# Optimization experiments

Hardware: AMD Instinct MI355X
Metric: run time of the kernel (lower is better)

Reference implementation:

```python
import jax, jax.numpy as jnp
import numpy as np

N_NODES = 100000
N_EDGES = 3200000
N_GRAPHS = 1000
F_IN = 3
H = 64


def setup_inputs() -> dict:
    key = jax.random.key(0)
    ks = jax.random.split(key, 12)
    x = jax.random.normal(ks[0], (N_NODES, F_IN), dtype=jnp.float32)
    edge_index = jax.random.randint(ks[1], (2, N_EDGES), 0, N_NODES, dtype=jnp.int64)
    batch = jnp.sort(jax.random.randint(ks[2], (N_NODES,), 0, N_GRAPHS, dtype=jnp.int64))
    def lin(k, fan_in, fan_out):
        bound = 1.0 / np.sqrt(fan_in)
        return jax.random.uniform(k, (fan_in, fan_out), jnp.float32, -bound, bound)
    return {
        "x": x,
        "edge_index": edge_index,
        "batch": batch,
        "eps1": jax.random.uniform(ks[3], (), jnp.float32),
        "eps2": jax.random.uniform(ks[4], (), jnp.float32),
        "eps3": jax.random.uniform(ks[5], (), jnp.float32),
        "W1": lin(ks[6], F_IN, H), "b1": jnp.zeros((H,), jnp.float32),
        "W2": lin(ks[7], H, H),    "b2": jnp.zeros((H,), jnp.float32),
        "W3": lin(ks[8], H, H),    "b3": jnp.zeros((H,), jnp.float32),
        "Wf1": lin(ks[9], H, 10),  "bf1": jnp.zeros((10,), jnp.float32),
        "Wf2": lin(ks[10], 10, 1), "bf2": jnp.zeros((1,), jnp.float32),
    }


def gin_conv(x, src, dst, eps, W, b):
    # GIN: out = nn((1+eps)*x + sum_{j in N(i)} x_j)
    agg = jax.ops.segment_sum(x[src], dst, num_segments=N_NODES)
    h = (1.0 + eps) * x + agg
    return h @ W + b


def reference(x, edge_index, batch, eps1, eps2, eps3, W1, b1, W2, b2, W3, b3, Wf1, bf1, Wf2, bf2):
    src, dst = edge_index[0], edge_index[1]
    h = jax.nn.relu(gin_conv(x, src, dst, eps1, W1, b1))
    h = jax.nn.relu(gin_conv(h, src, dst, eps2, W2, b2))
    h = jax.nn.relu(gin_conv(h, src, dst, eps3, W3, b3))
    # global mean pool over graphs
    sums = jax.ops.segment_sum(h, batch, num_segments=N_GRAPHS)
    counts = jax.ops.segment_sum(jnp.ones((N_NODES, 1), h.dtype), batch, num_segments=N_GRAPHS)
    pooled = sums / jnp.maximum(counts, 1.0)
    out = jax.nn.relu(pooled @ Wf1 + bf1)
    return out @ Wf2 + bf2
```

## Files before the change

kernel.cpp:

```cpp
#include <hip/hip_runtime.h>

#define N_NODES  100000
#define N_EDGES  3200000
#define N_GRAPHS 1000
#define HDIM     64

#define BUCK_LOG 8
#define BUCK_SZ  256
#define NBUCK    ((N_NODES + BUCK_SZ - 1) / BUCK_SZ)
#define CAP      16384
#define BIN_T    256
#define BIN_E    16
#define BIN_CHUNK (BIN_T * BIN_E)
#define CLUS_CAP 12288

typedef __attribute__((ext_vector_type(8))) short short8;
typedef __attribute__((ext_vector_type(4))) float f32x4;
typedef __attribute__((ext_vector_type(4))) int   int4v;


__device__ inline unsigned short f2bf(float v) {
    unsigned int b; __builtin_memcpy(&b, &v, 4);
    return (unsigned short)((b + 0x7FFFu + ((b >> 16) & 1u)) >> 16);
}
__device__ inline float bf2f(unsigned short u) {
    return __uint_as_float(((unsigned int)u) << 16);
}
__device__ inline void sth(unsigned short* p, float v) { *p = f2bf(v); }
__device__ inline float bflo(unsigned int d) { return __uint_as_float(d << 16); }
__device__ inline float bfhi(unsigned int d) { return __uint_as_float(d & 0xFFFF0000u); }

__device__ inline int clampi(int v, int lo, int hi) {
    return v < lo ? lo : (v > hi ? hi : v);
}


__global__ void k_zero(int* __restrict__ p, int n) {
    int i = blockIdx.x * blockDim.x + threadIdx.x;
    if (i < n) p[i] = 0;
}

__global__ void k_curinit(int* __restrict__ gcur) {
    int b = blockIdx.x * blockDim.x + threadIdx.x;
    if (b < NBUCK) gcur[b] = b * CAP;
}

__global__ void k_zrow(uint2* __restrict__ hA, uint2* __restrict__ hB) {
    int t = threadIdx.x;
    uint2 z; z.x = 0u; z.y = 0u;
    if (t < 16)       hA[(size_t)N_NODES * 16 + t] = z;
    else if (t < 32)  hB[(size_t)N_NODES * 16 + (t - 16)] = z;
}


__global__ __launch_bounds__(BIN_T) void k_bin(
        const int* __restrict__ ei, int* __restrict__ gcur,
        unsigned* __restrict__ pairs) {
    __shared__ int hist[NBUCK];
    __shared__ int base[NBUCK];
    for (int i = threadIdx.x; i < NBUCK; i += BIN_T) hist[i] = 0;
    __syncthreads();
    int e0 = blockIdx.x * BIN_CHUNK + threadIdx.x * BIN_E;
    int d[BIN_E], s[BIN_E];
    if (e0 + BIN_E <= N_EDGES) {
        const int4v* s4 = (const int4v*)ei;
        const int4v* d4 = (const int4v*)(ei + N_EDGES);
        #pragma unroll
        for (int q = 0; q < 4; ++q) {
            int4v dv = d4[(e0 >> 2) + q];
            int4v sv = s4[(e0 >> 2) + q];
            #pragma unroll
            for (int j = 0; j < 4; ++j) {
                d[q * 4 + j] = clampi(dv[j], 0, N_NODES - 1);
                s[q * 4 + j] = clampi(sv[j], 0, N_NODES - 1);
            }
        }
        #pragma unroll
        for (int k = 0; k < BIN_E; ++k) atomicAdd(&hist[d[k] >> BUCK_LOG], 1);
    } else {
        for (int k = 0; k < BIN_E; ++k) {
            int e = e0 + k;
            bool v = e < N_EDGES;
            d[k] = v ? clampi(ei[N_EDGES + e], 0, N_NODES - 1) : -1;
            s[k] = v ? clampi(ei[e], 0, N_NODES - 1) : 0;
            if (v) atomicAdd(&hist[d[k] >> BUCK_LOG], 1);
        }
    }
    __syncthreads();
    for (int i = threadIdx.x; i < NBUCK; i += BIN_T) {
        int c = hist[i];
        base[i] = c ? atomicAdd(&gcur[i], c) : 0;
        hist[i] = 0;
    }
    __syncthreads();
    #pragma unroll
    for (int k = 0; k < BIN_E; ++k) {
        if (d[k] >= 0) {
            int bk = d[k] >> BUCK_LOG;
            int r = atomicAdd(&hist[bk], 1);
            int idx = base[bk] + r;
            if (idx < (bk + 1) * CAP)
                pairs[idx] = ((unsigned)(d[k] & (BUCK_SZ - 1)) << 24) | (unsigned)s[k];
        }
    }
}

__global__ __launch_bounds__(512) void k_cluster(
        const unsigned* __restrict__ pairs, const int* __restrict__ gcur,
        int* __restrict__ poff, int* __restrict__ adj) {
    __shared__ int ladj[CLUS_CAP];
    __shared__ int lcur[BUCK_SZ];
    __shared__ int lsc[BUCK_SZ];
    __shared__ int ptot;
    int b  = blockIdx.x;
    int lo = b * BUCK_SZ;
    int nn = N_NODES - lo; if (nn > BUCK_SZ) nn = BUCK_SZ;
    int e0 = b * CAP;
    int cnt = gcur[b] - e0; if (cnt > CAP) cnt = CAP;
    int t = threadIdx.x;
    if (t < BUCK_SZ) lcur[t] = 0;
    __syncthreads();
    for (int i = t; i < cnt; i += 512) atomicAdd(&lcur[pairs[e0 + i] >> 24], 1);
    __syncthreads();
    int deg = 0, pdeg = 0;
    if (t < BUCK_SZ) {
        deg  = lcur[t];
        pdeg = (deg + 15) & ~15;
        if (pdeg > 2032) pdeg = 2032;
        lsc[t] = pdeg;
    }
    __syncthreads();
    #pragma unroll
    for (int d = 1; d < BUCK_SZ; d <<= 1) {
        int add = 0;
        if (t < BUCK_SZ && t >= d) add = lsc[t - d];
        __syncthreads();
        if (t < BUCK_SZ) lsc[t] += add;
        __syncthreads();
    }
    if (t == BUCK_SZ - 1) ptot = lsc[t];
    if (t < BUCK_SZ) {
        int exc = lsc[t] - pdeg;
        if (t < nn) poff[lo + t] = (e0 + exc) | ((pdeg >> 4) << 24);
        lcur[t] = exc;
    }
    __syncthreads();
    int pt = ptot;
    if (pt <= CLUS_CAP) {
        for (int i = t; i < pt; i += 512) ladj[i] = N_NODES;
        __syncthreads();
        for (int i = t; i < cnt; i += 512) {
            unsigned p = pairs[e0 + i];
            int pos = atomicAdd(&lcur[p >> 24], 1);
            ladj[pos] = (int)(p & 0xFFFFFFu);
        }
        __syncthreads();
        for (int i = t; i < pt; i += 512) adj[e0 + i] = ladj[i];
    } else {
        for (int i = t; i < pt && i < CAP + 4096; i += 512) adj[e0 + i] = N_NODES;
        __syncthreads();
        for (int i = t; i < cnt; i += 512) {
            unsigned p = pairs[e0 + i];
            int pos = atomicAdd(&lcur[p >> 24], 1);
            if (pos < CAP + 4096) adj[e0 + pos] = (int)(p & 0xFFFFFFu);
        }
    }
}


__global__ __launch_bounds__(256) void k_layer1(
        const float* __restrict__ x, const int* __restrict__ poff,
        const int* __restrict__ adj, const float* __restrict__ epsp,
        const float* __restrict__ W1, const float* __restrict__ b1,
        unsigned short* __restrict__ hout) {
    int wid  = (blockIdx.x * blockDim.x + threadIdx.x) >> 6;
    int lane = threadIdx.x & 63;
    if (wid >= N_NODES) return;
    int pk = poff[wid];
    int st = pk & 0xFFFFFF;
    int n16 = ((unsigned)pk >> 24) << 4;
    float a0 = 0.f, a1 = 0.f, a2 = 0.f;
    for (int e = lane; e < n16; e += 64) {
        int s = adj[st + e];
        bool ok = s < N_NODES;
        int sc = ok ? s : 0;
        float m = ok ? 1.f : 0.f;
        a0 += m * x[sc * 3 + 0];
        a1 += m * x[sc * 3 + 1];
        a2 += m * x[sc * 3 + 2];
    }
    #pragma unroll
    for (int d = 32; d; d >>= 1) {
        a0 += __shfl_xor(a0, d);
        a1 += __shfl_xor(a1, d);
        a2 += __shfl_xor(a2, d);
    }
    float ep = 1.0f + epsp[0];
    float s0 = ep * x[wid * 3 + 0] + a0;
    float s1 = ep * x[wid * 3 + 1] + a1;
    float s2 = ep * x[wid * 3 + 2] + a2;
    float o = b1[lane] + s0 * W1[lane] + s1 * W1[64 + lane] + s2 * W1[128 + lane];
    sth(&hout[(size_t)wid * 64 + lane], fmaxf(o, 0.f));
}


__global__ __launch_bounds__(256) void k_gemm(
        const unsigned short* __restrict__ hin, const float* __restrict__ W,
        unsigned short* __restrict__ Y) {
    int lane = threadIdx.x & 63;
    int r = lane & 15;
    int g = lane >> 4;
    int wave   = blockIdx.x * (blockDim.x >> 6) + (threadIdx.x >> 6);
    int nwaves = gridDim.x * (blockDim.x >> 6);

    short8 bh[2][4], bl[2][4];
    #pragma unroll
    for (int s = 0; s < 2; ++s) {
        #pragma unroll
        for (int t = 0; t < 4; ++t) {
            short8 hv, lv;
            #pragma unroll
            for (int i = 0; i < 8; ++i) {
                int k = s * 32 + g * 8 + i;
                int n = t * 16 + r;
                float w = W[k * 64 + n];
                unsigned short wh = f2bf(w);
                float whf = bf2f(wh);
                hv[i] = (short)wh;
                lv[i] = (short)f2bf(w - whf);
            }
            bh[s][t] = hv; bl[s][t] = lv;
        }
    }

    const int NT = N_NODES / 16;
    for (int mt = wave; mt < NT; mt += nwaves) {
        const unsigned short* arow = hin + (size_t)(mt * 16 + r) * 64;
        short8 a0 = *(const short8*)(arow + g * 8);
        short8 a1 = *(const short8*)(arow + 32 + g * 8);
        #pragma unroll
        for (int t = 0; t < 4; ++t) {
            f32x4 acc = {0.f, 0.f, 0.f, 0.f};
            acc = __builtin_amdgcn_mfma_f32_16x16x32_bf16(a0, bh[0][t], acc, 0, 0, 0);
            acc = __builtin_amdgcn_mfma_f32_16x16x32_bf16(a0, bl[0][t], acc, 0, 0, 0);
            acc = __builtin_amdgcn_mfma_f32_16x16x32_bf16(a1, bh[1][t], acc, 0, 0, 0);
            acc = __builtin_amdgcn_mfma_f32_16x16x32_bf16(a1, bl[1][t], acc, 0, 0, 0);
            #pragma unroll
            for (int j = 0; j < 4; ++j) {
                sth(&Y[(size_t)(mt * 16 + g * 4 + j) * 64 + t * 16 + r], acc[j]);
            }
        }
    }
}


__device__ inline void gather_node(
        const uint2* __restrict__ h2, int st, int nch,
        const int* __restrict__ adj, int sl, int g4,
        float& a0, float& a1, float& a2, float& a3) {
    for (int c = 0; c < nch; ++c) {
        int idxv = adj[st + (c << 4) + sl];
        uint2 dd[16];
        #pragma unroll
        for (int k = 0; k < 16; ++k) {
            int s = __shfl(idxv, (g4 << 4) + k);
            dd[k] = h2[(size_t)s * 16 + sl];
        }
        #pragma unroll
        for (int k = 0; k < 16; ++k) {
            a0 += bflo(dd[k].x); a1 += bfhi(dd[k].x);
            a2 += bflo(dd[k].y); a3 += bfhi(dd[k].y);
        }
    }
}

__global__ __launch_bounds__(512) void k_gather(
        const unsigned short* __restrict__ Y, const int* __restrict__ poff,
        const int* __restrict__ adj, const float* __restrict__ epsp,
        const float* __restrict__ b, unsigned short* __restrict__ hout) {
    int tid  = blockIdx.x * 512 + threadIdx.x;
    int node = tid >> 4;
    if (node >= N_NODES) return;
    int sl = threadIdx.x & 15;
    int g4 = (threadIdx.x >> 4) & 3;
    int pk = poff[node];
    int st = pk & 0xFFFFFF;
    int nch = (unsigned)pk >> 24;
    const uint2* h2 = (const uint2*)Y;
    float a0 = 0.f, a1 = 0.f, a2 = 0.f, a3 = 0.f;
    gather_node(h2, st, nch, adj, sl, g4, a0, a1, a2, a3);
    uint2 ds = h2[(size_t)node * 16 + sl];
    float ep = 1.0f + epsp[0];
    a0 = fmaxf(a0 + ep * bflo(ds.x) + b[4 * sl + 0], 0.f);
    a1 = fmaxf(a1 + ep * bfhi(ds.x) + b[4 * sl + 1], 0.f);
    a2 = fmaxf(a2 + ep * bflo(ds.y) + b[4 * sl + 2], 0.f);
    a3 = fmaxf(a3 + ep * bfhi(ds.y) + b[4 * sl + 3], 0.f);
    uint2 o;
    o.x = (unsigned int)f2bf(a0) | ((unsigned int)f2bf(a1) << 16);
    o.y = (unsigned int)f2bf(a2) | ((unsigned int)f2bf(a3) << 16);
    ((uint2*)hout)[(size_t)node * 16 + sl] = o;
}

__global__ __launch_bounds__(512) void k_gather_pool(
        const unsigned short* __restrict__ Y, const int* __restrict__ poff,
        const int* __restrict__ adj, const float* __restrict__ epsp,
        const float* __restrict__ b, const int* __restrict__ batch,
        float* __restrict__ pooled, int* __restrict__ cnt) {
    __shared__ float sacc[8 * 64];
    __shared__ int   scnt[8];
    for (int i = threadIdx.x; i < 8 * 64; i += 512) sacc[i] = 0.f;
    if (threadIdx.x < 8) scnt[threadIdx.x] = 0;
    __syncthreads();

    int tid  = blockIdx.x * 512 + threadIdx.x;
    int node = tid >> 4;
    int sl = threadIdx.x & 15;
    int g4 = (threadIdx.x >> 4) & 3;
    int g0 = clampi(batch[clampi(blockIdx.x * 32, 0, N_NODES - 1)], 0, N_GRAPHS - 1);

    if (node < N_NODES) {
        int pk = poff[node];
        int st = pk & 0xFFFFFF;
        int nch = (unsigned)pk >> 24;
        const uint2* h2 = (const uint2*)Y;
        float a0 = 0.f, a1 = 0.f, a2 = 0.f, a3 = 0.f;
        gather_node(h2, st, nch, adj, sl, g4, a0, a1, a2, a3);
        uint2 ds = h2[(size_t)node * 16 + sl];
        float ep = 1.0f + epsp[0];
        a0 = fmaxf(a0 + ep * bflo(ds.x) + b[4 * sl + 0], 0.f);
        a1 = fmaxf(a1 + ep * bfhi(ds.x) + b[4 * sl + 1], 0.f);
        a2 = fmaxf(a2 + ep * bflo(ds.y) + b[4 * sl + 2], 0.f);
        a3 = fmaxf(a3 + ep * bfhi(ds.y) + b[4 * sl + 3], 0.f);
        int g  = clampi(batch[node], 0, N_GRAPHS - 1);
        int og = g - g0;
        if (og >= 0 && og < 8) {
            atomicAdd(&sacc[og * 64 + 4 * sl + 0], a0);
            atomicAdd(&sacc[og * 64 + 4 * sl + 1], a1);
            atomicAdd(&sacc[og * 64 + 4 * sl + 2], a2);
            atomicAdd(&sacc[og * 64 + 4 * sl + 3], a3);
            if (sl == 0) atomicAdd(&scnt[og], 1);
        } else {
            atomicAdd(&pooled[g * 64 + 4 * sl + 0], a0);
            atomicAdd(&pooled[g * 64 + 4 * sl + 1], a1);
            atomicAdd(&pooled[g * 64 + 4 * sl + 2], a2);
            atomicAdd(&pooled[g * 64 + 4 * sl + 3], a3);
            if (sl == 0) atomicAdd(&cnt[g], 1);
        }
    }
    __syncthreads();
    int w = threadIdx.x >> 6;
    int lane = threadIdx.x & 63;
    if (w < 8) {
        int c = scnt[w];
        if (c > 0) {
            atomicAdd(&pooled[(g0 + w) * 64 + lane], sacc[w * 64 + lane]);
            if (lane == 0) atomicAdd(&cnt[g0 + w], c);
        }
    }
}


__global__ __launch_bounds__(256) void k_head(
        const float* __restrict__ pooled, const int* __restrict__ cnt,
        const float* __restrict__ Wf1, const float* __restrict__ bf1,
        const float* __restrict__ Wf2, const float* __restrict__ bf2,
        float* __restrict__ out) {
    int g = blockIdx.x * blockDim.x + threadIdx.x;
    if (g >= N_GRAPHS) return;
    float inv = 1.0f / fmaxf((float)cnt[g], 1.0f);
    float p[64];
    #pragma unroll
    for (int k = 0; k < 64; ++k) p[k] = pooled[g * 64 + k] * inv;
    float o = bf2[0];
    #pragma unroll
    for (int j = 0; j < 10; ++j) {
        float s = bf1[j];
        #pragma unroll
        for (int k = 0; k < 64; ++k) s += p[k] * Wf1[k * 10 + j];
        o += fmaxf(s, 0.f) * Wf2[j];
    }
    out[g] = o;
}


extern "C" void kernel_launch(void* const* d_in, const int* in_sizes, int n_in,
                              void* d_out, int out_size, void* d_ws, size_t ws_size,
                              hipStream_t stream) {
    const float* x     = (const float*)d_in[0];
    const int*   ei    = (const int*)d_in[1];
    const int*   batch = (const int*)d_in[2];
    const float* eps1 = (const float*)d_in[3];
    const float* eps2 = (const float*)d_in[4];
    const float* eps3 = (const float*)d_in[5];
    const float* W1 = (const float*)d_in[6];
    const float* b1 = (const float*)d_in[7];
    const float* W2 = (const float*)d_in[8];
    const float* b2 = (const float*)d_in[9];
    const float* W3 = (const float*)d_in[10];
    const float* b3 = (const float*)d_in[11];
    const float* Wf1 = (const float*)d_in[12];
    const float* bf1 = (const float*)d_in[13];
    const float* Wf2 = (const float*)d_in[14];
    const float* bf2 = (const float*)d_in[15];
    float* out = (float*)d_out;

    const size_t HROWS = (size_t)(N_NODES + 1) * HDIM;

    char* base = (char*)d_ws;
    unsigned short* hA = (unsigned short*)base;
    unsigned short* hB = (unsigned short*)(base + HROWS * 2);
    unsigned* pairs = (unsigned*)base;
    char* q = base + 2 * HROWS * 2;
    float* pooled = (float*)q;            q += 64000ull * 4;
    int*   cnt    = (int*)q;              q += 1000ull * 4;
    int*   poff   = (int*)q;              q += 100000ull * 4;
    int*   gcur   = (int*)q;              q += 512ull * 4;
    int*   adj    = (int*)q;

    const int TB = 256;
    k_curinit<<<(NBUCK + TB - 1) / TB, TB, 0, stream>>>(gcur);
    const int BINB = (N_EDGES + BIN_CHUNK - 1) / BIN_CHUNK;
    k_bin<<<BINB, BIN_T, 0, stream>>>(ei, gcur, pairs);
    k_cluster<<<NBUCK, 512, 0, stream>>>(pairs, gcur, poff, adj);

    k_zero<<<(65000 + TB - 1) / TB, TB, 0, stream>>>((int*)pooled, 65000);
    k_zrow<<<1, 64, 0, stream>>>((uint2*)hA, (uint2*)hB);

    const int L1_BLOCKS = (N_NODES * 64 + TB - 1) / TB;
    const int GB = (N_NODES * 16 + 511) / 512;

    k_layer1<<<L1_BLOCKS, TB, 0, stream>>>(x, poff, adj, eps1, W1, b1, hA);
    k_gemm<<<256, 256, 0, stream>>>(hA, W2, hB);
    k_gather<<<GB, 512, 0, stream>>>(hB, poff, adj, eps2, b2, hA);
    k_gemm<<<256, 256, 0, stream>>>(hA, W3, hB);
    k_gather_pool<<<GB, 512, 0, stream>>>(hB, poff, adj, eps3, b3, batch, pooled, cnt);

    k_head<<<(N_GRAPHS + TB - 1) / TB, TB, 0, stream>>>(pooled, cnt, Wf1, bf1, Wf2, bf2, out);
}
```

Before: 246.5 us.

## Split hidden features into four quarter planes and gather each quarter separately

The hidden activations move from a row-major [N,64] bf16 layout to four feature-quarter planes of [N,16], and the gemm and layer-1 writers are updated to match. The gather kernels now run one block per (16-node chunk, quarter). Each wave handles one node, its lanes split 16 neighbours by 4 feature slices, and partial sums are reduced across lanes with shuffles. The intent is that each quarter plane (about 3.2 MB) stays resident in L2/cache during its pass over the random neighbour reads. The cost is that adjacency and poff are read four times, and there are more cross-lane reductions and more pooling atomics.

```diff
diff --git a/kernel.cpp b/kernel.cpp
--- a/kernel.cpp
+++ b/kernel.cpp
@@ -1,9 +1,10 @@
 #include <hip/hip_runtime.h>
 
 #define N_NODES  100000
+#define N_GRAPHS 1000
 #define N_EDGES  3200000
-#define N_GRAPHS 1000
 #define HDIM     64
+#define NROWS    (N_NODES + 1)
 
 #define BUCK_LOG 8
 #define BUCK_SZ  256
@@ -48,8 +49,9 @@
 __global__ void k_zrow(uint2* __restrict__ hA, uint2* __restrict__ hB) {
     int t = threadIdx.x;
     uint2 z; z.x = 0u; z.y = 0u;
-    if (t < 16)       hA[(size_t)N_NODES * 16 + t] = z;
-    else if (t < 32)  hB[(size_t)N_NODES * 16 + (t - 16)] = z;
+    if (t < 16)       hA[((size_t)(t >> 2) * NROWS + N_NODES) * 4 + (t & 3)] = z;
+    else if (t < 32) { int u = t - 16;
+                      hB[((size_t)(u >> 2) * NROWS + N_NODES) * 4 + (u & 3)] = z; }
 }
 
 
@@ -200,7 +202,7 @@
     float s1 = ep * x[wid * 3 + 1] + a1;
     float s2 = ep * x[wid * 3 + 2] + a2;
     float o = b1[lane] + s0 * W1[lane] + s1 * W1[64 + lane] + s2 * W1[128 + lane];
-    sth(&hout[(size_t)wid * 64 + lane], fmaxf(o, 0.f));
+    hout[((size_t)(lane >> 4) * NROWS + wid) * 16 + (lane & 15)] = f2bf(fmaxf(o, 0.f));
 }
 
 
@@ -235,9 +237,9 @@
 
     const int NT = N_NODES / 16;
     for (int mt = wave; mt < NT; mt += nwaves) {
-        const unsigned short* arow = hin + (size_t)(mt * 16 + r) * 64;
-        short8 a0 = *(const short8*)(arow + g * 8);
-        short8 a1 = *(const short8*)(arow + 32 + g * 8);
+        int row = mt * 16 + r;
+        short8 a0 = *(const short8*)(hin + ((size_t)(g >> 1) * NROWS + row) * 16 + (g & 1) * 8);
+        short8 a1 = *(const short8*)(hin + ((size_t)(2 + (g >> 1)) * NROWS + row) * 16 + (g & 1) * 8);
         #pragma unroll
         for (int t = 0; t < 4; ++t) {
             f32x4 acc = {0.f, 0.f, 0.f, 0.f};
@@ -247,114 +249,123 @@
             acc = __builtin_amdgcn_mfma_f32_16x16x32_bf16(a1, bl[1][t], acc, 0, 0, 0);
             #pragma unroll
             for (int j = 0; j < 4; ++j) {
-                sth(&Y[(size_t)(mt * 16 + g * 4 + j) * 64 + t * 16 + r], acc[j]);
+                sth(&Y[((size_t)t * NROWS + mt * 16 + g * 4 + j) * 16 + r], acc[j]);
             }
         }
     }
 }
 
 
-__device__ inline void gather_node(
-        const uint2* __restrict__ h2, int st, int nch,
-        const int* __restrict__ adj, int sl, int g4,
+__device__ inline void gather_q(
+        const uint2* __restrict__ h2, size_t qbase, int st, int nch,
+        const int* __restrict__ adj, int kg, int fq,
         float& a0, float& a1, float& a2, float& a3) {
     for (int c = 0; c < nch; ++c) {
-        int idxv = adj[st + (c << 4) + sl];
-        uint2 dd[16];
-        #pragma unroll
-        for (int k = 0; k < 16; ++k) {
-            int s = __shfl(idxv, (g4 << 4) + k);
-            dd[k] = h2[(size_t)s * 16 + sl];
-        }
-        #pragma unroll
-        for (int k = 0; k < 16; ++k) {
-            a0 += bflo(dd[k].x); a1 += bfhi(dd[k].x);
-            a2 += bflo(dd[k].y); a3 += bfhi(dd[k].y);
-        }
-    }
-}
-
-__global__ __launch_bounds__(512) void k_gather(
+        int s = __builtin_nontemporal_load(adj + st + (c << 4) + kg);
+        uint2 d = h2[qbase + (size_t)s * 4 + fq];
+        a0 += bflo(d.x); a1 += bfhi(d.x);
+        a2 += bflo(d.y); a3 += bfhi(d.y);
+    }
+    #pragma unroll
+    for (int m = 4; m <= 32; m <<= 1) {
+        a0 += __shfl_xor(a0, m);
+        a1 += __shfl_xor(a1, m);
+        a2 += __shfl_xor(a2, m);
+        a3 += __shfl_xor(a3, m);
+    }
+}
+
+__global__ __launch_bounds__(1024) void k_gather(
         const unsigned short* __restrict__ Y, const int* __restrict__ poff,
         const int* __restrict__ adj, const float* __restrict__ epsp,
         const float* __restrict__ b, unsigned short* __restrict__ hout) {
-    int tid  = blockIdx.x * 512 + threadIdx.x;
-    int node = tid >> 4;
-    if (node >= N_NODES) return;
-    int sl = threadIdx.x & 15;
-    int g4 = (threadIdx.x >> 4) & 3;
+    int q     = blockIdx.x & 3;
+    int chunk = blockIdx.x >> 2;
+    int node  = chunk * 16 + (threadIdx.x >> 6);
+    int lane  = threadIdx.x & 63;
     int pk = poff[node];
     int st = pk & 0xFFFFFF;
     int nch = (unsigned)pk >> 24;
     const uint2* h2 = (const uint2*)Y;
+    size_t qbase = (size_t)q * NROWS * 4;
     float a0 = 0.f, a1 = 0.f, a2 = 0.f, a3 = 0.f;
-    gather_node(h2, st, nch, adj, sl, g4, a0, a1, a2, a3);
-    uint2 ds = h2[(size_t)node * 16 + sl];
-    float ep = 1.0f + epsp[0];
-    a0 = fmaxf(a0 + ep * bflo(ds.x) + b[4 * sl + 0], 0.f);
-    a1 = fmaxf(a1 + ep * bfhi(ds.x) + b[4 * sl + 1], 0.f);
-    a2 = fmaxf(a2 + ep * bflo(ds.y) + b[4 * sl + 2], 0.f);
-    a3 = fmaxf(a3 + ep * bfhi(ds.y) + b[4 * sl + 3], 0.f);
-    uint2 o;
-    o.x = (unsigned int)f2bf(a0) | ((unsigned int)f2bf(a1) << 16);
-    o.y = (unsigned int)f2bf(a2) | ((unsigned int)f2bf(a3) << 16);
-    ((uint2*)hout)[(size_t)node * 16 + sl] = o;
-}
-
-__global__ __launch_bounds__(512) void k_gather_pool(
+    gather_q(h2, qbase, st, nch, adj, lane >> 2, lane & 3, a0, a1, a2, a3);
+    if (lane < 4) {
+        uint2 ds = h2[qbase + (size_t)node * 4 + lane];
+        float ep = 1.0f + epsp[0];
+        int fb = q * 16 + lane * 4;
+        a0 = fmaxf(a0 + ep * bflo(ds.x) + b[fb + 0], 0.f);
+        a1 = fmaxf(a1 + ep * bfhi(ds.x) + b[fb + 1], 0.f);
+        a2 = fmaxf(a2 + ep * bflo(ds.y) + b[fb + 2], 0.f);
+        a3 = fmaxf(a3 + ep * bfhi(ds.y) + b[fb + 3], 0.f);
+        unsigned lo32 = (unsigned)f2bf(a0) | ((unsigned)f2bf(a1) << 16);
+        unsigned hi32 = (unsigned)f2bf(a2) | ((unsigned)f2bf(a3) << 16);
+        unsigned long long pk8 = ((unsigned long long)hi32 << 32) | lo32;
+        __builtin_nontemporal_store(pk8,
+            (unsigned long long*)hout + qbase + (size_t)node * 4 + lane);
+    }
+}
+
+__global__ __launch_bounds__(1024) void k_gather_pool(
         const unsigned short* __restrict__ Y, const int* __restrict__ poff,
         const int* __restrict__ adj, const float* __restrict__ epsp,
         const float* __restrict__ b, const int* __restrict__ batch,
         float* __restrict__ pooled, int* __restrict__ cnt) {
-    __shared__ float sacc[8 * 64];
+    __shared__ float sacc[8 * 16];
     __shared__ int   scnt[8];
-    for (int i = threadIdx.x; i < 8 * 64; i += 512) sacc[i] = 0.f;
+    if (threadIdx.x < 128) sacc[threadIdx.x] = 0.f;
     if (threadIdx.x < 8) scnt[threadIdx.x] = 0;
     __syncthreads();
 
-    int tid  = blockIdx.x * 512 + threadIdx.x;
-    int node = tid >> 4;
-    int sl = threadIdx.x & 15;
-    int g4 = (threadIdx.x >> 4) & 3;
-    int g0 = clampi(batch[clampi(blockIdx.x * 32, 0, N_NODES - 1)], 0, N_GRAPHS - 1);
-
-    if (node < N_NODES) {
-        int pk = poff[node];
-        int st = pk & 0xFFFFFF;
-        int nch = (unsigned)pk >> 24;
-        const uint2* h2 = (const uint2*)Y;
-        float a0 = 0.f, a1 = 0.f, a2 = 0.f, a3 = 0.f;
-        gather_node(h2, st, nch, adj, sl, g4, a0, a1, a2, a3);
-        uint2 ds = h2[(size_t)node * 16 + sl];
+    int q     = blockIdx.x & 3;
+    int chunk = blockIdx.x >> 2;
+    int node  = chunk * 16 + (threadIdx.x >> 6);
+    int lane  = threadIdx.x & 63;
+    int pk = poff[node];
+    int st = pk & 0xFFFFFF;
+    int nch = (unsigned)pk >> 24;
+    const uint2* h2 = (const uint2*)Y;
+    size_t qbase = (size_t)q * NROWS * 4;
+    float a0 = 0.f, a1 = 0.f, a2 = 0.f, a3 = 0.f;
+    gather_q(h2, qbase, st, nch, adj, lane >> 2, lane & 3, a0, a1, a2, a3);
+
+    int g  = clampi(batch[node], 0, N_GRAPHS - 1);
+    int g0 = clampi(batch[chunk * 16], 0, N_GRAPHS - 1);
+    int og = g - g0;
+    if (lane < 4) {
+        uint2 ds = h2[qbase + (size_t)node * 4 + lane];
         float ep = 1.0f + epsp[0];
-        a0 = fmaxf(a0 + ep * bflo(ds.x) + b[4 * sl + 0], 0.f);
-        a1 = fmaxf(a1 + ep * bfhi(ds.x) + b[4 * sl + 1], 0.f);
-        a2 = fmaxf(a2 + ep * bflo(ds.y) + b[4 * sl + 2], 0.f);
-        a3 = fmaxf(a3 + ep * bfhi(ds.y) + b[4 * sl + 3], 0.f);
-        int g  = clampi(batch[node], 0, N_GRAPHS - 1);
-        int og = g - g0;
+        int fb = q * 16 + lane * 4;
+        a0 = fmaxf(a0 + ep * bflo(ds.x) + b[fb + 0], 0.f);
+        a1 = fmaxf(a1 + ep * bfhi(ds.x) + b[fb + 1], 0.f);
+        a2 = fmaxf(a2 + ep * bflo(ds.y) + b[fb + 2], 0.f);
+        a3 = fmaxf(a3 + ep * bfhi(ds.y) + b[fb + 3], 0.f);
         if (og >= 0 && og < 8) {
-            atomicAdd(&sacc[og * 64 + 4 * sl + 0], a0);
-            atomicAdd(&sacc[og * 64 + 4 * sl + 1], a1);
-            atomicAdd(&sacc[og * 64 + 4 * sl + 2], a2);
-            atomicAdd(&sacc[og * 64 + 4 * sl + 3], a3);
-            if (sl == 0) atomicAdd(&scnt[og], 1);
+            atomicAdd(&sacc[og * 16 + lane * 4 + 0], a0);
+            atomicAdd(&sacc[og * 16 + lane * 4 + 1], a1);
+            atomicAdd(&sacc[og * 16 + lane * 4 + 2], a2);
+            atomicAdd(&sacc[og * 16 + lane * 4 + 3], a3);
         } else {
-            atomicAdd(&pooled[g * 64 + 4 * sl + 0], a0);
-            atomicAdd(&pooled[g * 64 + 4 * sl + 1], a1);
-            atomicAdd(&pooled[g * 64 + 4 * sl + 2], a2);
-            atomicAdd(&pooled[g * 64 + 4 * sl + 3], a3);
-            if (sl == 0) atomicAdd(&cnt[g], 1);
-        }
+            atomicAdd(&pooled[g * 64 + q * 16 + lane * 4 + 0], a0);
+            atomicAdd(&pooled[g * 64 + q * 16 + lane * 4 + 1], a1);
+            atomicAdd(&pooled[g * 64 + q * 16 + lane * 4 + 2], a2);
+            atomicAdd(&pooled[g * 64 + q * 16 + lane * 4 + 3], a3);
+        }
+    }
+    if (q == 0 && lane == 0) {
+        if (og >= 0 && og < 8) atomicAdd(&scnt[og], 1);
+        else atomicAdd(&cnt[g], 1);
     }
     __syncthreads();
     int w = threadIdx.x >> 6;
-    int lane = threadIdx.x & 63;
     if (w < 8) {
-        int c = scnt[w];
-        if (c > 0) {
-            atomicAdd(&pooled[(g0 + w) * 64 + lane], sacc[w * 64 + lane]);
-            if (lane == 0) atomicAdd(&cnt[g0 + w], c);
+        if (lane < 16) {
+            float v = sacc[w * 16 + lane];
+            if (v != 0.f) atomicAdd(&pooled[(g0 + w) * 64 + q * 16 + lane], v);
+        }
+        if (q == 0 && lane == 0) {
+            int c = scnt[w];
+            if (c > 0) atomicAdd(&cnt[g0 + w], c);
         }
     }
 }
@@ -404,13 +415,13 @@
     const float* bf2 = (const float*)d_in[15];
     float* out = (float*)d_out;
 
-    const size_t HROWS = (size_t)(N_NODES + 1) * HDIM;
+    const size_t HBYTES = (size_t)NROWS * HDIM * 2;
 
     char* base = (char*)d_ws;
     unsigned short* hA = (unsigned short*)base;
-    unsigned short* hB = (unsigned short*)(base + HROWS * 2);
+    unsigned short* hB = (unsigned short*)(base + HBYTES);
     unsigned* pairs = (unsigned*)base;
-    char* q = base + 2 * HROWS * 2;
+    char* q = base + 2 * HBYTES;
     float* pooled = (float*)q;            q += 64000ull * 4;
     int*   cnt    = (int*)q;              q += 1000ull * 4;
     int*   poff   = (int*)q;              q += 100000ull * 4;
@@ -427,13 +438,13 @@
     k_zrow<<<1, 64, 0, stream>>>((uint2*)hA, (uint2*)hB);
 
     const int L1_BLOCKS = (N_NODES * 64 + TB - 1) / TB;
-    const int GB = (N_NODES * 16 + 511) / 512;
+    const int GQB = (N_NODES / 16) * 4;
 
     k_layer1<<<L1_BLOCKS, TB, 0, stream>>>(x, poff, adj, eps1, W1, b1, hA);
     k_gemm<<<256, 256, 0, stream>>>(hA, W2, hB);
-    k_gather<<<GB, 512, 0, stream>>>(hB, poff, adj, eps2, b2, hA);
+    k_gather<<<GQB, 1024, 0, stream>>>(hB, poff, adj, eps2, b2, hA);
     k_gemm<<<256, 256, 0, stream>>>(hA, W3, hB);
-    k_gather_pool<<<GB, 512, 0, stream>>>(hB, poff, adj, eps3, b3, batch, pooled, cnt);
+    k_gather_pool<<<GQB, 1024, 0, stream>>>(hB, poff, adj, eps3, b3, batch, pooled, cnt);
 
     k_head<<<(N_GRAPHS + TB - 1) / TB, TB, 0, stream>>>(pooled, cnt, Wf1, bf1, Wf2, bf2, out);
 }
```

Result: slower. 491.5 us (+99.4%).
